# Optimization experiments

Hardware: AMD Instinct MI355X
Metric: run time of the kernel (lower is better)

The kernel has to match this reference:

```python
import jax, jax.numpy as jnp
import numpy as np

ALPHA = 0.2  # LeakyReLU negative slope


def setup_inputs() -> dict:
    key = jax.random.key(0)
    k1, k2 = jax.random.split(key)
    B, N, Fin, Fout = 4, 4096, 256, 128
    h = jax.random.normal(k1, (B, N, Fin), dtype=jnp.float32)
    adj = jnp.zeros((B, N, N), dtype=bool)  # unused by the original forward
    # Linear(in,out,bias=False); stored as [in,out] for h @ W
    W = jax.random.normal(k2, (Fin, Fout), dtype=jnp.float32) * (1.0 / np.sqrt(Fin))
    return {"h": h, "adj": adj, "W": W}


def reference(h, adj, W):
    # h: [B,N,Fin], W: [Fin,Fout]
    hp = jnp.einsum("bnf,fo->bno", h, W)                    # [B,N,Fout]
    e = jnp.einsum("bnd,bmd->bnm", hp, hp)                  # [B,N,N]
    e = jnp.where(e >= 0, e, ALPHA * e)                      # LeakyReLU
    attn = jax.nn.softmax(e, axis=1)                         # softmax over dim=1 (rows)
    # torch: sum_j( hp[b,i] * attn[b,i,j] ) == hp[b,i] * sum_j attn[b,i,j]
    row_mass = jnp.sum(attn, axis=2, keepdims=True)          # [B,N,1]
    return hp * row_mass
```

## Files before the change

### kernel.cpp

```cpp
#include <hip/hip_runtime.h>
#include <hip/hip_bf16.h>

#define ALPHA 0.2f

constexpr int BN   = 4;
constexpr int NN   = 4096;
constexpr int FIN  = 256;
constexpr int FOUT = 128;
constexpr int NSPLIT = 4;

typedef __attribute__((ext_vector_type(8))) short bf16x8;
typedef __attribute__((ext_vector_type(4))) float f32x4;

#define MFMA16(a, b, c) __builtin_amdgcn_mfma_f32_16x16x32_bf16((a), (b), (c), 0, 0, 0)

__device__ __forceinline__ void split8(const float* x, uint4& H, uint4& L) {
    ushort hb[8], lb[8];
    #pragma unroll
    for (int i = 0; i < 8; ++i) {
        float xv = x[i];
        __hip_bfloat16 hh = __float2bfloat16(xv);
        float hf = __bfloat162float(hh);
        __hip_bfloat16 lw = __float2bfloat16(xv - hf);
        hb[i] = reinterpret_cast<const ushort&>(hh);
        lb[i] = reinterpret_cast<const ushort&>(lw);
    }
    H = make_uint4((uint)hb[0] | ((uint)hb[1] << 16), (uint)hb[2] | ((uint)hb[3] << 16),
                   (uint)hb[4] | ((uint)hb[5] << 16), (uint)hb[6] | ((uint)hb[7] << 16));
    L = make_uint4((uint)lb[0] | ((uint)lb[1] << 16), (uint)lb[2] | ((uint)lb[3] << 16),
                   (uint)lb[4] | ((uint)lb[5] << 16), (uint)lb[6] | ((uint)lb[7] << 16));
}

template<int ROWS, int KGSH>
__device__ __forceinline__ void stage_split(const float* __restrict__ src, int strideF,
                                            ushort* hi, ushort* lo, int tid) {
    constexpr int KG = 1 << KGSH;
    #pragma unroll
    for (int idx = tid; idx < ROWS * KG; idx += 256) {
        int row = idx >> KGSH, g = idx & (KG - 1);
        const float4* p4 = reinterpret_cast<const float4*>(src + (size_t)row * strideF + g * 8);
        float4 u = p4[0], v = p4[1];
        float x[8] = {u.x, u.y, u.z, u.w, v.x, v.y, v.z, v.w};
        uint4 H, L;
        split8(x, H, L);
        int gran = (row << KGSH) + (g ^ (row & 7));
        reinterpret_cast<uint4*>(hi)[gran] = H;
        reinterpret_cast<uint4*>(lo)[gran] = L;
    }
}

template<int ROWS, int KGSH>
__device__ __forceinline__ void stage_copy(const ushort* __restrict__ src, int strideU,
                                           ushort* dst, int tid) {
    constexpr int KG = 1 << KGSH;
    #pragma unroll
    for (int idx = tid; idx < ROWS * KG; idx += 256) {
        int row = idx >> KGSH, g = idx & (KG - 1);
        uint4 vv = *reinterpret_cast<const uint4*>(src + (size_t)row * strideU + g * 8);
        reinterpret_cast<uint4*>(dst)[(row << KGSH) + (g ^ (row & 7))] = vv;
    }
}

__device__ __forceinline__ bf16x8 frag16(const ushort* s, int rowbase, int kstep, int kgsh, int lane) {
    int r = rowbase + (lane & 15);
    int g = kstep * 4 + (lane >> 4);
    int gran = (r << kgsh) + (g ^ (r & 7));
    return *reinterpret_cast<const bf16x8*>(s + gran * 8);
}

__global__ void k_prepW(const float* __restrict__ W, ushort* __restrict__ Wt_hi,
                        ushort* __restrict__ Wt_lo) {
    int idx = blockIdx.x * 256 + threadIdx.x;
    if (idx >= FOUT * (FIN / 8)) return;
    int n = idx >> 5, g = idx & 31;
    float x[8];
    #pragma unroll
    for (int i = 0; i < 8; ++i) x[i] = W[(size_t)(g * 8 + i) * FOUT + n];
    uint4 H, L;
    split8(x, H, L);
    reinterpret_cast<uint4*>(Wt_hi)[n * 32 + g] = H;
    reinterpret_cast<uint4*>(Wt_lo)[n * 32 + g] = L;
}

__global__ __launch_bounds__(256)
void k_hp(const float* __restrict__ h, const ushort* __restrict__ Wt_hi,
          const ushort* __restrict__ Wt_lo, float* __restrict__ hp) {
    __shared__ __align__(16) ushort Ah[64 * 64], Al[64 * 64];
    __shared__ __align__(16) ushort Bh[128 * 64], Bl[128 * 64];
    const int tid = threadIdx.x, lane = tid & 63, wid = tid >> 6;
    const int wy = wid >> 1, wx = wid & 1;
    const int ibase = blockIdx.x * 64;
    f32x4 z = {0.f, 0.f, 0.f, 0.f};
    f32x4 acc[2][4] = {{z, z, z, z}, {z, z, z, z}};
    for (int kt = 0; kt < 4; ++kt) {
        __syncthreads();
        stage_split<64, 3>(h + (size_t)ibase * FIN + kt * 64, FIN, Ah, Al, tid);
        stage_copy<128, 3>(Wt_hi + kt * 64, FIN, Bh, tid);
        stage_copy<128, 3>(Wt_lo + kt * 64, FIN, Bl, tid);
        __syncthreads();
        #pragma unroll
        for (int pr = 0; pr < 3; ++pr) {
            const ushort* A = (pr == 2) ? Al : Ah;
            const ushort* B = (pr == 1) ? Bl : Bh;
            #pragma unroll
            for (int ks = 0; ks < 2; ++ks) {
                bf16x8 a0 = frag16(A, wy * 32, ks, 3, lane);
                bf16x8 a1 = frag16(A, wy * 32 + 16, ks, 3, lane);
                #pragma unroll
                for (int c = 0; c < 4; ++c) {
                    bf16x8 bb = frag16(B, wx * 64 + c * 16, ks, 3, lane);
                    acc[0][c] = MFMA16(a0, bb, acc[0][c]);
                    acc[1][c] = MFMA16(a1, bb, acc[1][c]);
                }
            }
        }
    }
    #pragma unroll
    for (int r = 0; r < 2; ++r)
        #pragma unroll
        for (int c = 0; c < 4; ++c)
            #pragma unroll
            for (int p = 0; p < 4; ++p) {
                int row = ibase + wy * 32 + r * 16 + (lane >> 4) * 4 + p;
                int col = wx * 64 + c * 16 + (lane & 15);
                hp[(size_t)row * FOUT + col] = acc[r][c][p];
            }
}

__device__ __forceinline__ void etile(const ushort* Ihi, const ushort* Ilo,
                                      const ushort* Jhi, const ushort* Jlo,
                                      int wy, int wx, int lane, f32x4 acc[2][2]) {
    #pragma unroll
    for (int pr = 0; pr < 3; ++pr) {
        const ushort* A = (pr == 2) ? Ilo : Ihi;
        const ushort* B = (pr == 1) ? Jlo : Jhi;
        #pragma unroll
        for (int ks = 0; ks < 4; ++ks) {
            bf16x8 a0 = frag16(A, wy * 32, ks, 4, lane);
            bf16x8 a1 = frag16(A, wy * 32 + 16, ks, 4, lane);
            bf16x8 b0 = frag16(B, wx * 32, ks, 4, lane);
            bf16x8 b1 = frag16(B, wx * 32 + 16, ks, 4, lane);
            acc[0][0] = MFMA16(a0, b0, acc[0][0]);
            acc[0][1] = MFMA16(a0, b1, acc[0][1]);
            acc[1][0] = MFMA16(a1, b0, acc[1][0]);
            acc[1][1] = MFMA16(a1, b1, acc[1][1]);
        }
    }
}

__device__ __forceinline__ void decode_bid(int bid, int& b, int& strip, int& q) {
    int slot = bid & 7;
    b = slot >> 1;
    int sub = ((bid >> 3) << 1) | (slot & 1);
    strip = sub >> 2;
    q = sub & 3;
}

__global__ __launch_bounds__(256)
void k_colstats(const float* __restrict__ hp, float* __restrict__ m_part,
                float* __restrict__ s_part) {
    __shared__ __align__(16) ushort Jhi[64 * 128], Jlo[64 * 128];
    __shared__ __align__(16) ushort Ihi[64 * 128], Ilo[64 * 128];
    const int tid = threadIdx.x, lane = tid & 63, wid = tid >> 6;
    const int wy = wid >> 1, wx = wid & 1;
    int b, strip, iq;
    decode_bid(blockIdx.x, b, strip, iq);
    const int jbase = strip * 64;
    const float* hpb = hp + (size_t)b * NN * FOUT;
    stage_split<64, 4>(hpb + (size_t)jbase * FOUT, FOUT, Jhi, Jlo, tid);
    float mrun[2] = {-1e30f, -1e30f}, srun[2] = {0.f, 0.f};
    for (int t = 0; t < (NN / NSPLIT) / 64; ++t) {
        int ibase = iq * (NN / NSPLIT) + t * 64;
        __syncthreads();
        stage_split<64, 4>(hpb + (size_t)ibase * FOUT, FOUT, Ihi, Ilo, tid);
        __syncthreads();
        f32x4 zz = {0.f, 0.f, 0.f, 0.f};
        f32x4 acc[2][2] = {{zz, zz}, {zz, zz}};
        etile(Ihi, Ilo, Jhi, Jlo, wy, wx, lane, acc);
        #pragma unroll
        for (int c = 0; c < 2; ++c) {
            float tm = -1e30f;
            #pragma unroll
            for (int r = 0; r < 2; ++r)
                #pragma unroll
                for (int p = 0; p < 4; ++p) {
                    float x = acc[r][c][p];
                    float g = fmaxf(x, ALPHA * x);
                    acc[r][c][p] = g;
                    tm = fmaxf(tm, g);
                }
            tm = fmaxf(tm, __shfl_xor(tm, 16));
            tm = fmaxf(tm, __shfl_xor(tm, 32));
            float mnew = fmaxf(mrun[c], tm);
            float ss = 0.f;
            #pragma unroll
            for (int r = 0; r < 2; ++r)
                #pragma unroll
                for (int p = 0; p < 4; ++p) ss += __expf(acc[r][c][p] - mnew);
            ss += __shfl_xor(ss, 16);
            ss += __shfl_xor(ss, 32);
            srun[c] = srun[c] * __expf(mrun[c] - mnew) + ss;
            mrun[c] = mnew;
        }
    }
    if (lane < 16) {
        int set = ((b * NSPLIT + iq) << 1) + wy;
        #pragma unroll
        for (int c = 0; c < 2; ++c) {
            int j = jbase + wx * 32 + c * 16 + lane;
            m_part[(size_t)set * NN + j] = mrun[c];
            s_part[(size_t)set * NN + j] = srun[c];
        }
    }
}

__global__ void k_merge(const float* __restrict__ m_part, const float* __restrict__ s_part,
                        float* __restrict__ m_fin, float* __restrict__ inv_s) {
    int idx = blockIdx.x * 256 + threadIdx.x;
    if (idx >= BN * NN) return;
    int b = idx >> 12, j = idx & (NN - 1);
    float M = -1e30f;
    #pragma unroll
    for (int k = 0; k < 2 * NSPLIT; ++k)
        M = fmaxf(M, m_part[(size_t)(b * 2 * NSPLIT + k) * NN + j]);
    float S = 0.f;
    #pragma unroll
    for (int k = 0; k < 2 * NSPLIT; ++k) {
        float mp = m_part[(size_t)(b * 2 * NSPLIT + k) * NN + j];
        float sp = s_part[(size_t)(b * 2 * NSPLIT + k) * NN + j];
        S += sp * __expf(mp - M);
    }
    m_fin[idx] = M;
    inv_s[idx] = 1.f / S;
}

__global__ __launch_bounds__(256)
void k_rowsum(const float* __restrict__ hp, const float* __restrict__ m_fin,
              const float* __restrict__ inv_s, float* __restrict__ rs_part) {
    __shared__ __align__(16) ushort Ihi[64 * 128], Ilo[64 * 128];
    __shared__ __align__(16) ushort Jhi[64 * 128], Jlo[64 * 128];
    __shared__ float red[64][2];
    const int tid = threadIdx.x, lane = tid & 63, wid = tid >> 6;
    const int wy = wid >> 1, wx = wid & 1;
    int b, strip, jq;
    decode_bid(blockIdx.x, b, strip, jq);
    const int ibase = strip * 64;
    const float* hpb = hp + (size_t)b * NN * FOUT;
    stage_split<64, 4>(hpb + (size_t)ibase * FOUT, FOUT, Ihi, Ilo, tid);
    float rsum[2][4] = {{0.f, 0.f, 0.f, 0.f}, {0.f, 0.f, 0.f, 0.f}};
    for (int t = 0; t < (NN / NSPLIT) / 64; ++t) {
        int jb = jq * (NN / NSPLIT) + t * 64;
        __syncthreads();
        stage_split<64, 4>(hpb + (size_t)jb * FOUT, FOUT, Jhi, Jlo, tid);
        __syncthreads();
        f32x4 zz = {0.f, 0.f, 0.f, 0.f};
        f32x4 acc[2][2] = {{zz, zz}, {zz, zz}};
        etile(Ihi, Ilo, Jhi, Jlo, wy, wx, lane, acc);
        float mj[2], isj[2];
        #pragma unroll
        for (int c = 0; c < 2; ++c) {
            int j = jb + wx * 32 + c * 16 + (lane & 15);
            mj[c] = m_fin[(size_t)b * NN + j];
            isj[c] = inv_s[(size_t)b * NN + j];
        }
        #pragma unroll
        for (int r = 0; r < 2; ++r)
            #pragma unroll
            for (int p = 0; p < 4; ++p) {
                float s0 = 0.f;
                #pragma unroll
                for (int c = 0; c < 2; ++c) {
                    float x = acc[r][c][p];
                    float g = fmaxf(x, ALPHA * x);
                    s0 += __expf(g - mj[c]) * isj[c];
                }
                rsum[r][p] += s0;
            }
    }
    #pragma unroll
    for (int r = 0; r < 2; ++r)
        #pragma unroll
        for (int p = 0; p < 4; ++p) {
            float v = rsum[r][p];
            v += __shfl_xor(v, 1);
            v += __shfl_xor(v, 2);
            v += __shfl_xor(v, 4);
            v += __shfl_xor(v, 8);
            if ((lane & 15) == 0) red[wy * 32 + r * 16 + (lane >> 4) * 4 + p][wx] = v;
        }
    __syncthreads();
    if (tid < 64)
        rs_part[(size_t)(b * NSPLIT + jq) * NN + ibase + tid] = red[tid][0] + red[tid][1];
}

__global__ void k_scale(const float* __restrict__ rs_part, float* __restrict__ out) {
    int idx = blockIdx.x * 256 + threadIdx.x;
    if (idx >= BN * NN * FOUT / 4) return;
    int row = idx >> 5;
    int b = row >> 12, i = row & (NN - 1);
    float rm = 0.f;
    #pragma unroll
    for (int k = 0; k < NSPLIT; ++k)
        rm += rs_part[(size_t)(b * NSPLIT + k) * NN + i];
    float4 v = reinterpret_cast<float4*>(out)[idx];
    v.x *= rm; v.y *= rm; v.z *= rm; v.w *= rm;
    reinterpret_cast<float4*>(out)[idx] = v;
}

extern "C" void kernel_launch(void* const* d_in, const int* in_sizes, int n_in,
                              void* d_out, int out_size, void* d_ws, size_t ws_size,
                              hipStream_t stream) {
    (void)in_sizes; (void)n_in; (void)out_size; (void)ws_size;
    const float* h = (const float*)d_in[0];
    const float* W = (const float*)d_in[2];
    float* out = (float*)d_out;
    ushort* Wt_hi = (ushort*)d_ws;
    ushort* Wt_lo = Wt_hi + FOUT * FIN;
    float* m_part = (float*)(Wt_lo + FOUT * FIN);
    float* s_part = m_part + BN * 2 * NSPLIT * NN;
    float* m_fin  = s_part + BN * 2 * NSPLIT * NN;
    float* inv_s  = m_fin + BN * NN;
    float* rs_part = inv_s + BN * NN;

    k_prepW<<<(FOUT * (FIN / 8) + 255) / 256, 256, 0, stream>>>(W, Wt_hi, Wt_lo);
    k_hp<<<BN * NN / 64, 256, 0, stream>>>(h, Wt_hi, Wt_lo, out);
    k_colstats<<<NSPLIT * BN * (NN / 64), 256, 0, stream>>>(out, m_part, s_part);
    k_merge<<<(BN * NN + 255) / 256, 256, 0, stream>>>(m_part, s_part, m_fin, inv_s);
    k_rowsum<<<NSPLIT * BN * (NN / 64), 256, 0, stream>>>(out, m_fin, inv_s, rs_part);
    k_scale<<<(BN * NN * FOUT / 4 + 255) / 256, 256, 0, stream>>>(rs_part, out);
}
```

Baseline: 499.4 us.

## Precompute bf16 hi/lo split of hp and enlarge attention tiles to 128x128

k_hp now also writes bf16 hi/lo halves of hp to workspace, so the colstats and rowsum kernels copy presplit data instead of re-splitting fp32 tiles on every stage. Both kernels move from 64x64 to 128x128 tiles, with each wave computing a 4x4 grid of MFMA fragments, and the query split changes from 4 to 8. This raises register and fragment reuse and cuts the number of global and shared loads. In exchange, shared memory per block grows to 128KB, which limits occupancy, and register pressure rises from 16 accumulators per wave.

```diff
diff --git a/kernel.cpp b/kernel.cpp
--- a/kernel.cpp
+++ b/kernel.cpp
@@ -7,7 +7,7 @@
 constexpr int NN   = 4096;
 constexpr int FIN  = 256;
 constexpr int FOUT = 128;
-constexpr int NSPLIT = 4;
+constexpr int NQ   = 8;
 
 typedef __attribute__((ext_vector_type(8))) short bf16x8;
 typedef __attribute__((ext_vector_type(4))) float f32x4;
@@ -84,7 +84,8 @@
 
 __global__ __launch_bounds__(256)
 void k_hp(const float* __restrict__ h, const ushort* __restrict__ Wt_hi,
-          const ushort* __restrict__ Wt_lo, float* __restrict__ hp) {
+          const ushort* __restrict__ Wt_lo, float* __restrict__ hp,
+          ushort* __restrict__ hp_hi, ushort* __restrict__ hp_lo) {
     __shared__ __align__(16) ushort Ah[64 * 64], Al[64 * 64];
     __shared__ __align__(16) ushort Bh[128 * 64], Bl[128 * 64];
     const int tid = threadIdx.x, lane = tid & 63, wid = tid >> 6;
@@ -123,28 +124,41 @@
             for (int p = 0; p < 4; ++p) {
                 int row = ibase + wy * 32 + r * 16 + (lane >> 4) * 4 + p;
                 int col = wx * 64 + c * 16 + (lane & 15);
-                hp[(size_t)row * FOUT + col] = acc[r][c][p];
+                float x = acc[r][c][p];
+                __hip_bfloat16 hh = __float2bfloat16(x);
+                float hf = __bfloat162float(hh);
+                __hip_bfloat16 lw = __float2bfloat16(x - hf);
+                size_t off = (size_t)row * FOUT + col;
+                hp[off] = x;
+                hp_hi[off] = reinterpret_cast<const ushort&>(hh);
+                hp_lo[off] = reinterpret_cast<const ushort&>(lw);
             }
 }
 
-__device__ __forceinline__ void etile(const ushort* Ihi, const ushort* Ilo,
-                                      const ushort* Jhi, const ushort* Jlo,
-                                      int wy, int wx, int lane, f32x4 acc[2][2]) {
-    #pragma unroll
-    for (int pr = 0; pr < 3; ++pr) {
-        const ushort* A = (pr == 2) ? Ilo : Ihi;
-        const ushort* B = (pr == 1) ? Jlo : Jhi;
-        #pragma unroll
-        for (int ks = 0; ks < 4; ++ks) {
-            bf16x8 a0 = frag16(A, wy * 32, ks, 4, lane);
-            bf16x8 a1 = frag16(A, wy * 32 + 16, ks, 4, lane);
-            bf16x8 b0 = frag16(B, wx * 32, ks, 4, lane);
-            bf16x8 b1 = frag16(B, wx * 32 + 16, ks, 4, lane);
-            acc[0][0] = MFMA16(a0, b0, acc[0][0]);
-            acc[0][1] = MFMA16(a0, b1, acc[0][1]);
-            acc[1][0] = MFMA16(a1, b0, acc[1][0]);
-            acc[1][1] = MFMA16(a1, b1, acc[1][1]);
-        }
+__device__ __forceinline__ void etile44(const ushort* Ihi, const ushort* Ilo,
+                                        const ushort* Jhi, const ushort* Jlo,
+                                        int wy, int wx, int lane, f32x4 acc[4][4]) {
+    #pragma unroll
+    for (int ks = 0; ks < 4; ++ks) {
+        bf16x8 aH[4], aL[4], bH[4], bL[4];
+        #pragma unroll
+        for (int r = 0; r < 4; ++r) {
+            aH[r] = frag16(Ihi, wy * 64 + r * 16, ks, 4, lane);
+            aL[r] = frag16(Ilo, wy * 64 + r * 16, ks, 4, lane);
+        }
+        #pragma unroll
+        for (int c = 0; c < 4; ++c) {
+            bH[c] = frag16(Jhi, wx * 64 + c * 16, ks, 4, lane);
+            bL[c] = frag16(Jlo, wx * 64 + c * 16, ks, 4, lane);
+        }
+        #pragma unroll
+        for (int r = 0; r < 4; ++r)
+            #pragma unroll
+            for (int c = 0; c < 4; ++c) {
+                acc[r][c] = MFMA16(aH[r], bH[c], acc[r][c]);
+                acc[r][c] = MFMA16(aH[r], bL[c], acc[r][c]);
+                acc[r][c] = MFMA16(aL[r], bH[c], acc[r][c]);
+            }
     }
 }
 
@@ -152,36 +166,44 @@
     int slot = bid & 7;
     b = slot >> 1;
     int sub = ((bid >> 3) << 1) | (slot & 1);
-    strip = sub >> 2;
-    q = sub & 3;
+    strip = sub >> 3;
+    q = sub & 7;
 }
 
 __global__ __launch_bounds__(256)
-void k_colstats(const float* __restrict__ hp, float* __restrict__ m_part,
-                float* __restrict__ s_part) {
-    __shared__ __align__(16) ushort Jhi[64 * 128], Jlo[64 * 128];
-    __shared__ __align__(16) ushort Ihi[64 * 128], Ilo[64 * 128];
+void k_colstats(const ushort* __restrict__ hp_hi, const ushort* __restrict__ hp_lo,
+                float* __restrict__ m_part, float* __restrict__ s_part) {
+    __shared__ __align__(16) ushort Jhi[128 * 128], Jlo[128 * 128];
+    __shared__ __align__(16) ushort Ihi[128 * 128], Ilo[128 * 128];
     const int tid = threadIdx.x, lane = tid & 63, wid = tid >> 6;
     const int wy = wid >> 1, wx = wid & 1;
-    int b, strip, iq;
-    decode_bid(blockIdx.x, b, strip, iq);
-    const int jbase = strip * 64;
-    const float* hpb = hp + (size_t)b * NN * FOUT;
-    stage_split<64, 4>(hpb + (size_t)jbase * FOUT, FOUT, Jhi, Jlo, tid);
-    float mrun[2] = {-1e30f, -1e30f}, srun[2] = {0.f, 0.f};
-    for (int t = 0; t < (NN / NSPLIT) / 64; ++t) {
-        int ibase = iq * (NN / NSPLIT) + t * 64;
-        __syncthreads();
-        stage_split<64, 4>(hpb + (size_t)ibase * FOUT, FOUT, Ihi, Ilo, tid);
+    int b, strip, q;
+    decode_bid(blockIdx.x, b, strip, q);
+    const int jbase = strip * 128;
+    const ushort* hb_hi = hp_hi + (size_t)b * NN * FOUT;
+    const ushort* hb_lo = hp_lo + (size_t)b * NN * FOUT;
+    stage_copy<128, 4>(hb_hi + (size_t)jbase * FOUT, FOUT, Jhi, tid);
+    stage_copy<128, 4>(hb_lo + (size_t)jbase * FOUT, FOUT, Jlo, tid);
+    float mrun[4] = {-1e30f, -1e30f, -1e30f, -1e30f};
+    float srun[4] = {0.f, 0.f, 0.f, 0.f};
+    for (int t = 0; t < 4; ++t) {
+        int ibase = q * 512 + t * 128;
+        __syncthreads();
+        stage_copy<128, 4>(hb_hi + (size_t)ibase * FOUT, FOUT, Ihi, tid);
+        stage_copy<128, 4>(hb_lo + (size_t)ibase * FOUT, FOUT, Ilo, tid);
         __syncthreads();
         f32x4 zz = {0.f, 0.f, 0.f, 0.f};
-        f32x4 acc[2][2] = {{zz, zz}, {zz, zz}};
-        etile(Ihi, Ilo, Jhi, Jlo, wy, wx, lane, acc);
-        #pragma unroll
-        for (int c = 0; c < 2; ++c) {
+        f32x4 acc[4][4];
+        #pragma unroll
+        for (int r = 0; r < 4; ++r)
+            #pragma unroll
+            for (int c = 0; c < 4; ++c) acc[r][c] = zz;
+        etile44(Ihi, Ilo, Jhi, Jlo, wy, wx, lane, acc);
+        #pragma unroll
+        for (int c = 0; c < 4; ++c) {
             float tm = -1e30f;
             #pragma unroll
-            for (int r = 0; r < 2; ++r)
+            for (int r = 0; r < 4; ++r)
                 #pragma unroll
                 for (int p = 0; p < 4; ++p) {
                     float x = acc[r][c][p];
@@ -194,7 +216,7 @@
             float mnew = fmaxf(mrun[c], tm);
             float ss = 0.f;
             #pragma unroll
-            for (int r = 0; r < 2; ++r)
+            for (int r = 0; r < 4; ++r)
                 #pragma unroll
                 for (int p = 0; p < 4; ++p) ss += __expf(acc[r][c][p] - mnew);
             ss += __shfl_xor(ss, 16);
@@ -204,10 +226,10 @@
         }
     }
     if (lane < 16) {
-        int set = ((b * NSPLIT + iq) << 1) + wy;
-        #pragma unroll
-        for (int c = 0; c < 2; ++c) {
-            int j = jbase + wx * 32 + c * 16 + lane;
+        int set = b * 16 + q * 2 + wy;
+        #pragma unroll
+        for (int c = 0; c < 4; ++c) {
+            int j = jbase + wx * 64 + c * 16 + lane;
             m_part[(size_t)set * NN + j] = mrun[c];
             s_part[(size_t)set * NN + j] = srun[c];
         }
@@ -221,13 +243,13 @@
     int b = idx >> 12, j = idx & (NN - 1);
     float M = -1e30f;
     #pragma unroll
-    for (int k = 0; k < 2 * NSPLIT; ++k)
-        M = fmaxf(M, m_part[(size_t)(b * 2 * NSPLIT + k) * NN + j]);
+    for (int k = 0; k < 16; ++k)
+        M = fmaxf(M, m_part[(size_t)(b * 16 + k) * NN + j]);
     float S = 0.f;
     #pragma unroll
-    for (int k = 0; k < 2 * NSPLIT; ++k) {
-        float mp = m_part[(size_t)(b * 2 * NSPLIT + k) * NN + j];
-        float sp = s_part[(size_t)(b * 2 * NSPLIT + k) * NN + j];
+    for (int k = 0; k < 16; ++k) {
+        float mp = m_part[(size_t)(b * 16 + k) * NN + j];
+        float sp = s_part[(size_t)(b * 16 + k) * NN + j];
         S += sp * __expf(mp - M);
     }
     m_fin[idx] = M;
@@ -235,41 +257,49 @@
 }
 
 __global__ __launch_bounds__(256)
-void k_rowsum(const float* __restrict__ hp, const float* __restrict__ m_fin,
-              const float* __restrict__ inv_s, float* __restrict__ rs_part) {
-    __shared__ __align__(16) ushort Ihi[64 * 128], Ilo[64 * 128];
-    __shared__ __align__(16) ushort Jhi[64 * 128], Jlo[64 * 128];
-    __shared__ float red[64][2];
+void k_rowsum(const ushort* __restrict__ hp_hi, const ushort* __restrict__ hp_lo,
+              const float* __restrict__ m_fin, const float* __restrict__ inv_s,
+              float* __restrict__ rs_part) {
+    __shared__ __align__(16) ushort Ihi[128 * 128], Ilo[128 * 128];
+    __shared__ __align__(16) ushort Jhi[128 * 128], Jlo[128 * 128];
+    __shared__ float red[128][2];
     const int tid = threadIdx.x, lane = tid & 63, wid = tid >> 6;
     const int wy = wid >> 1, wx = wid & 1;
     int b, strip, jq;
     decode_bid(blockIdx.x, b, strip, jq);
-    const int ibase = strip * 64;
-    const float* hpb = hp + (size_t)b * NN * FOUT;
-    stage_split<64, 4>(hpb + (size_t)ibase * FOUT, FOUT, Ihi, Ilo, tid);
-    float rsum[2][4] = {{0.f, 0.f, 0.f, 0.f}, {0.f, 0.f, 0.f, 0.f}};
-    for (int t = 0; t < (NN / NSPLIT) / 64; ++t) {
-        int jb = jq * (NN / NSPLIT) + t * 64;
-        __syncthreads();
-        stage_split<64, 4>(hpb + (size_t)jb * FOUT, FOUT, Jhi, Jlo, tid);
-        __syncthreads();
-        f32x4 zz = {0.f, 0.f, 0.f, 0.f};
-        f32x4 acc[2][2] = {{zz, zz}, {zz, zz}};
-        etile(Ihi, Ilo, Jhi, Jlo, wy, wx, lane, acc);
-        float mj[2], isj[2];
-        #pragma unroll
-        for (int c = 0; c < 2; ++c) {
-            int j = jb + wx * 32 + c * 16 + (lane & 15);
+    const int ibase = strip * 128;
+    const ushort* hb_hi = hp_hi + (size_t)b * NN * FOUT;
+    const ushort* hb_lo = hp_lo + (size_t)b * NN * FOUT;
+    stage_copy<128, 4>(hb_hi + (size_t)ibase * FOUT, FOUT, Ihi, tid);
+    stage_copy<128, 4>(hb_lo + (size_t)ibase * FOUT, FOUT, Ilo, tid);
+    float rsum[4][4] = {};
+    for (int t = 0; t < 4; ++t) {
+        int jb = jq * 512 + t * 128;
+        __syncthreads();
+        stage_copy<128, 4>(hb_hi + (size_t)jb * FOUT, FOUT, Jhi, tid);
+        stage_copy<128, 4>(hb_lo + (size_t)jb * FOUT, FOUT, Jlo, tid);
+        __syncthreads();
+        float mj[4], isj[4];
+        #pragma unroll
+        for (int c = 0; c < 4; ++c) {
+            int j = jb + wx * 64 + c * 16 + (lane & 15);
             mj[c] = m_fin[(size_t)b * NN + j];
             isj[c] = inv_s[(size_t)b * NN + j];
         }
-        #pragma unroll
-        for (int r = 0; r < 2; ++r)
+        f32x4 zz = {0.f, 0.f, 0.f, 0.f};
+        f32x4 acc[4][4];
+        #pragma unroll
+        for (int r = 0; r < 4; ++r)
+            #pragma unroll
+            for (int c = 0; c < 4; ++c) acc[r][c] = zz;
+        etile44(Ihi, Ilo, Jhi, Jlo, wy, wx, lane, acc);
+        #pragma unroll
+        for (int r = 0; r < 4; ++r)
             #pragma unroll
             for (int p = 0; p < 4; ++p) {
                 float s0 = 0.f;
                 #pragma unroll
-                for (int c = 0; c < 2; ++c) {
+                for (int c = 0; c < 4; ++c) {
                     float x = acc[r][c][p];
                     float g = fmaxf(x, ALPHA * x);
                     s0 += __expf(g - mj[c]) * isj[c];
@@ -278,7 +308,7 @@
             }
     }
     #pragma unroll
-    for (int r = 0; r < 2; ++r)
+    for (int r = 0; r < 4; ++r)
         #pragma unroll
         for (int p = 0; p < 4; ++p) {
             float v = rsum[r][p];
@@ -286,11 +316,11 @@
             v += __shfl_xor(v, 2);
             v += __shfl_xor(v, 4);
             v += __shfl_xor(v, 8);
-            if ((lane & 15) == 0) red[wy * 32 + r * 16 + (lane >> 4) * 4 + p][wx] = v;
+            if ((lane & 15) == 0) red[wy * 64 + r * 16 + (lane >> 4) * 4 + p][wx] = v;
         }
     __syncthreads();
-    if (tid < 64)
-        rs_part[(size_t)(b * NSPLIT + jq) * NN + ibase + tid] = red[tid][0] + red[tid][1];
+    if (tid < 128)
+        rs_part[(size_t)(b * NQ + jq) * NN + ibase + tid] = red[tid][0] + red[tid][1];
 }
 
 __global__ void k_scale(const float* __restrict__ rs_part, float* __restrict__ out) {
@@ -300,8 +330,8 @@
     int b = row >> 12, i = row & (NN - 1);
     float rm = 0.f;
     #pragma unroll
-    for (int k = 0; k < NSPLIT; ++k)
-        rm += rs_part[(size_t)(b * NSPLIT + k) * NN + i];
+    for (int k = 0; k < NQ; ++k)
+        rm += rs_part[(size_t)(b * NQ + k) * NN + i];
     float4 v = reinterpret_cast<float4*>(out)[idx];
     v.x *= rm; v.y *= rm; v.z *= rm; v.w *= rm;
     reinterpret_cast<float4*>(out)[idx] = v;
@@ -314,18 +344,20 @@
     const float* h = (const float*)d_in[0];
     const float* W = (const float*)d_in[2];
     float* out = (float*)d_out;
-    ushort* Wt_hi = (ushort*)d_ws;
+    ushort* hp_hi = (ushort*)d_ws;
+    ushort* hp_lo = hp_hi + (size_t)BN * NN * FOUT;
+    ushort* Wt_hi = hp_lo + (size_t)BN * NN * FOUT;
     ushort* Wt_lo = Wt_hi + FOUT * FIN;
     float* m_part = (float*)(Wt_lo + FOUT * FIN);
-    float* s_part = m_part + BN * 2 * NSPLIT * NN;
-    float* m_fin  = s_part + BN * 2 * NSPLIT * NN;
-    float* inv_s  = m_fin + BN * NN;
-    float* rs_part = inv_s + BN * NN;
+    float* s_part = m_part + (size_t)BN * 16 * NN;
+    float* m_fin  = s_part + (size_t)BN * 16 * NN;
+    float* inv_s  = m_fin + (size_t)BN * NN;
+    float* rs_part = inv_s + (size_t)BN * NN;
 
     k_prepW<<<(FOUT * (FIN / 8) + 255) / 256, 256, 0, stream>>>(W, Wt_hi, Wt_lo);
-    k_hp<<<BN * NN / 64, 256, 0, stream>>>(h, Wt_hi, Wt_lo, out);
-    k_colstats<<<NSPLIT * BN * (NN / 64), 256, 0, stream>>>(out, m_part, s_part);
+    k_hp<<<BN * NN / 64, 256, 0, stream>>>(h, Wt_hi, Wt_lo, out, hp_hi, hp_lo);
+    k_colstats<<<BN * NQ * (NN / 128), 256, 0, stream>>>(hp_hi, hp_lo, m_part, s_part);
     k_merge<<<(BN * NN + 255) / 256, 256, 0, stream>>>(m_part, s_part, m_fin, inv_s);
-    k_rowsum<<<NSPLIT * BN * (NN / 64), 256, 0, stream>>>(out, m_fin, inv_s, rs_part);
+    k_rowsum<<<BN * NQ * (NN / 128), 256, 0, stream>>>(hp_hi, hp_lo, m_fin, inv_s, rs_part);
     k_scale<<<(BN * NN * FOUT / 4 + 255) / 256, 256, 0, stream>>>(rs_part, out);
 }
```

New measurement: 498.5 us. No clear change (-0.2%).
